# Performance work log

Hardware: AMD Instinct MI355X
Metric: run time of the kernel (lower is better)

Reference implementation:

```python
import jax, jax.numpy as jnp
import numpy as np

B, H, S, D = 2, 12, 4096, 768
BS = 64              # block size
HD = D // H          # head dim = 64
NB = S // BS         # 64 blocks
MC = 3               # max graph connections per block
PEN = -10000.0
RSQRT_D = 1.0 / np.sqrt(HD).astype(np.float32)


def setup_inputs() -> dict:
    key = jax.random.key(0)
    ks = jax.random.split(key, 6)
    hidden_states = jax.random.normal(ks[0], (B, S, D), jnp.float32)
    Wq = jax.random.normal(ks[1], (D, D), jnp.float32) * 0.02
    Wk = jax.random.normal(ks[2], (D, D), jnp.float32) * 0.02
    Wv = jax.random.normal(ks[3], (D, D), jnp.float32) * 0.02
    Wo = jax.random.normal(ks[4], (D, D), jnp.float32) * 0.02
    graph_attn = jax.random.randint(ks[5], (B, H, NB, MC), 0, NB, jnp.int32)
    return dict(
        hidden_states=hidden_states, Wq=Wq, Wk=Wk, Wv=Wv, Wo=Wo,
        band_mask=jnp.ones((B, 1, NB - 4, BS, 3 * BS), jnp.float32),
        from_mask=jnp.ones((B, 1, S, 1), jnp.float32),
        to_mask=jnp.ones((B, 1, 1, S), jnp.float32),
        from_blocked_mask=jnp.ones((B, NB, BS), jnp.float32),
        to_blocked_mask=jnp.ones((B, NB, BS), jnp.float32),
        graph_attn=graph_attn,
    )


def reference(hidden_states, Wq, Wk, Wv, Wo, band_mask, from_mask, to_mask,
              from_blocked_mask, to_blocked_mask, graph_attn):
    def proj(W):  # [B,S,D] -> [B,H,S,HD]
        return (hidden_states @ W.T).reshape(B, S, H, HD).transpose(0, 2, 1, 3)

    q, k, v = proj(Wq), proj(Wk), proj(Wv)
    bq = q.reshape(B, H, NB, BS, HD)
    bk = k.reshape(B, H, NB, BS, HD)
    bv = v.reshape(B, H, NB, BS, HD)

    # gather graph-selected key/value blocks: [B,H,NB,MC*BS,HD]
    gather = jax.vmap(jax.vmap(lambda blocks, idx: blocks[idx]))
    gk = gather(bk, graph_attn).reshape(B, H, NB, MC * BS, HD)
    gv = gather(bv, graph_attn).reshape(B, H, NB, MC * BS, HD)

    # graph mask from blocked masks: [B,H,NB,BS,MC*BS]
    gm = jax.vmap(lambda tm, ga: tm[ga])(to_blocked_mask, graph_attn)  # [B,H,NB,MC,BS]
    gm = gm.reshape(B, H, NB, MC * BS)
    graph_mask = jnp.einsum('blq,bhlk->bhlqk', from_blocked_mask, gm)

    # ---- first block: global attention over all keys ----
    fp = jnp.einsum('bhqd,bhkd->bhqk', bq[:, :, 0], k) * RSQRT_D + (1.0 - to_mask) * PEN
    first_ctx = jnp.einsum('bhqk,bhkd->bhqd', jax.nn.softmax(fp, -1), v)[:, :, None]

    # ---- second block: blocks 0,1,2,last + graph-gathered ----
    sk = jnp.concatenate([bk[:, :, 0], bk[:, :, 1], bk[:, :, 2], bk[:, :, -1], gk[:, :, 1]], axis=2)
    sv = jnp.concatenate([bv[:, :, 0], bv[:, :, 1], bv[:, :, 2], bv[:, :, -1], gv[:, :, 1]], axis=2)
    sp = jnp.einsum('bhqd,bhkd->bhqk', bq[:, :, 1], sk) * RSQRT_D
    seq_pad = jnp.concatenate([to_mask[:, :, :, :3 * BS], to_mask[:, :, :, -BS:],
                               jnp.ones((B, 1, 1, MC * BS), to_mask.dtype)], axis=3)
    rand_pad = jnp.concatenate([jnp.ones((B, H, BS, 4 * BS), graph_mask.dtype),
                                graph_mask[:, :, 1]], axis=3)
    sp = sp + (1.0 - jnp.minimum(seq_pad, rand_pad)) * PEN
    second_ctx = jnp.einsum('bhqk,bhkd->bhqd', jax.nn.softmax(sp, -1), sv)[:, :, None]

    # ---- middle blocks: sliding window (3 blocks) + first + last + graph ----
    ek = jnp.concatenate([bk[:, :, 1:-3], bk[:, :, 2:-2], bk[:, :, 3:-1]], axis=3)  # [B,H,NB-4,3BS,HD]
    ev = jnp.concatenate([bv[:, :, 1:-3], bv[:, :, 2:-2], bv[:, :, 3:-1]], axis=3)
    qm = bq[:, :, 2:-2]
    inner = jnp.einsum('bhlqd,bhlkd->bhlqk', qm, ek) * RSQRT_D + (1.0 - band_mask) * PEN
    randp = jnp.einsum('bhlqd,bhlkd->bhlqk', qm, gk[:, :, 2:-2]) * RSQRT_D + (1.0 - graph_mask[:, :, 2:-2]) * PEN
    firstp = jnp.einsum('bhlqd,bhkd->bhlqk', qm, bk[:, :, 0]) * RSQRT_D + (1.0 - to_mask[:, :, :, None, :BS]) * PEN
    lastp = jnp.einsum('bhlqd,bhkd->bhlqk', qm, bk[:, :, -1]) * RSQRT_D + (1.0 - to_mask[:, :, :, None, -BS:]) * PEN
    band = jnp.concatenate([firstp, inner, randp, lastp], axis=-1)
    attn = jax.nn.softmax(band, -1)
    mid_ctx = (jnp.einsum('bhlqk,bhlkd->bhlqd', attn[..., BS:4 * BS], ev)
               + jnp.einsum('bhlqk,bhlkd->bhlqd', attn[..., 4 * BS:4 * BS + MC * BS], gv[:, :, 2:-2])
               + jnp.einsum('bhlqk,bhkd->bhlqd', attn[..., :BS], bv[:, :, 0])
               + jnp.einsum('bhlqk,bhkd->bhlqd', attn[..., -BS:], bv[:, :, -1]))

    # ---- second-to-last block ----
    slk = jnp.concatenate([bk[:, :, 0], bk[:, :, -3], bk[:, :, -2], bk[:, :, -1], gk[:, :, -2]], axis=2)
    slv = jnp.concatenate([bv[:, :, 0], bv[:, :, -3], bv[:, :, -2], bv[:, :, -1], gv[:, :, -2]], axis=2)
    slp = jnp.einsum('bhqd,bhkd->bhqk', bq[:, :, -2], slk) * RSQRT_D
    sl_seq = jnp.concatenate([to_mask[:, :, :, :BS], to_mask[:, :, :, -3 * BS:],
                              jnp.ones((B, 1, 1, MC * BS), to_mask.dtype)], axis=3)
    sl_rand = jnp.concatenate([jnp.ones((B, H, BS, 4 * BS), graph_mask.dtype),
                               graph_mask[:, :, -2]], axis=3)
    slp = slp + (1.0 - jnp.minimum(sl_seq, sl_rand)) * PEN
    sl_ctx = jnp.einsum('bhqk,bhkd->bhqd', jax.nn.softmax(slp, -1), slv)[:, :, None]

    # ---- last block: global attention over all keys ----
    lp = jnp.einsum('bhqd,bhkd->bhqk', bq[:, :, -1], k) * RSQRT_D + (1.0 - to_mask) * PEN
    last_ctx = jnp.einsum('bhqk,bhkd->bhqd', jax.nn.softmax(lp, -1), v)[:, :, None]

    ctx = jnp.concatenate([first_ctx, second_ctx, mid_ctx, sl_ctx, last_ctx], axis=2)
    ctx = ctx.reshape(B, H, S, HD) * from_mask            # [B,H,S,HD]
    ctx = ctx.transpose(0, 2, 1, 3).reshape(B, S, D)      # [B,S,D]
    return ctx @ Wo.T                                     # output projection (no bias)
```

## Files before the change

### kernel.cpp

```cpp
#include <hip/hip_runtime.h>
#include <hip/hip_bf16.h>

#define BB 2
#define HH 12
#define SS 4096
#define DD 768
#define HD 64
#define NBK 64
#define MC 3

typedef __attribute__((ext_vector_type(8))) short short8_t;
typedef __attribute__((ext_vector_type(4))) float float4_t;

__device__ __forceinline__ unsigned short f2bf(float f) {
  union { float f; unsigned u; } c;
  c.f = f;
  unsigned u = c.u + 0x7FFFu + ((c.u >> 16) & 1u);
  return (unsigned short)(u >> 16);
}

__device__ __forceinline__ void gload16(const unsigned short* gp,
                                        unsigned short* lp) {
  __builtin_amdgcn_global_load_lds(
      (const __attribute__((address_space(1))) unsigned int*)gp,
      (__attribute__((address_space(3))) unsigned int*)lp, 16, 0, 0);
}

#define LDK 72

__global__ __launch_bounds__(256) void cvt_all(
    const float* __restrict__ hs, const float* __restrict__ Wq,
    const float* __restrict__ Wk, const float* __restrict__ Wv,
    const float* __restrict__ Wo, unsigned short* __restrict__ hsb,
    unsigned short* __restrict__ wqkvb, unsigned short* __restrict__ wob) {
  long i4 = (long)blockIdx.x * 256 + threadIdx.x;
  const float* src;
  unsigned short* dst;
  if (i4 < 1572864) {
    src = hs + i4 * 4;
    dst = hsb + i4 * 4;
  } else {
    long r = i4 - 1572864;
    int w = (int)(r / 147456);
    long e = r % 147456;
    src = (w == 0 ? Wq : w == 1 ? Wk : w == 2 ? Wv : Wo) + e * 4;
    dst = (w < 3) ? (wqkvb + (long)w * 589824 + e * 4) : (wob + e * 4);
  }
  float4_t v = *(const float4_t*)src;
  uint2 p;
  p.x = (unsigned)f2bf(v[0]) | ((unsigned)f2bf(v[1]) << 16);
  p.y = (unsigned)f2bf(v[2]) | ((unsigned)f2bf(v[3]) << 16);
  *(uint2*)dst = p;
}

#define STAGE_A(buf_, A_, m0_, kt_)                                           \
  {                                                                           \
    int rr_ = lane >> 3;                                                      \
    int cg_ = (lane & 7) ^ rr_;                                               \
    _Pragma("unroll") for (int u = 0; u < 4; u++) {                           \
      int g_ = w * 4 + u;                                                     \
      gload16(A_ + (size_t)(m0_ + g_ * 8 + rr_) * DD + kt_ + cg_ * 8,         \
              &As[buf_][g_ * 512]);                                           \
    }                                                                         \
  }

#define LOAD_FRAGS_AB(buf_, kt_, kk_)                                         \
  int cb = qd + ((kk_) >> 3);                                                 \
  short8_t af[4], bfr[4];                                                     \
  _Pragma("unroll") for (int i = 0; i < 4; i++) {                             \
    int r_ = wm + i * 16 + fr;                                                \
    af[i] = *(const short8_t*)&As[buf_][r_ * 64 + (cb ^ (fr & 7)) * 8];       \
  }                                                                           \
  _Pragma("unroll") for (int j = 0; j < 4; j++)                               \
    bfr[j] = *(const short8_t*)&Wg[(size_t)(j * 16) * DD + (kt_) + (kk_)];

__global__ __launch_bounds__(256) void gemm_qkv_b(
    const unsigned short* __restrict__ A, const unsigned short* __restrict__ W,
    unsigned short* __restrict__ qb, unsigned short* __restrict__ kb,
    unsigned short* __restrict__ vtb) {
  __shared__ unsigned short As[2][128 * 64];
  int tid = threadIdx.x;
  int m0 = blockIdx.x * 128;
  int n0 = blockIdx.y * 128;
  int lane = tid & 63;
  int w = tid >> 6;
  int wm = (w >> 1) * 64;
  int wn = (w & 1) * 64;
  int fr = lane & 15;
  int qd = lane >> 4;
  int ysel = n0 / 768;
  const unsigned short* Wg = W + (size_t)(n0 + wn + fr) * DD + qd * 8;

  float4_t acc[4][4];
#pragma unroll
  for (int i = 0; i < 4; i++)
#pragma unroll
    for (int j = 0; j < 4; j++)
#pragma unroll
      for (int r = 0; r < 4; r++) acc[i][j][r] = 0.f;

  STAGE_A(0, A, m0, 0)
  int p = 0;

  if (ysel < 2) {
    for (int kt = 0; kt < DD; kt += 64) {
      __syncthreads();
      if (kt + 64 < DD) STAGE_A(p ^ 1, A, m0, kt + 64)
#pragma unroll
      for (int kk = 0; kk < 64; kk += 32) {
        LOAD_FRAGS_AB(p, kt, kk)
#pragma unroll
        for (int i = 0; i < 4; i++)
#pragma unroll
          for (int j = 0; j < 4; j++)
            acc[j][i] = __builtin_amdgcn_mfma_f32_16x16x32_bf16(
                bfr[j], af[i], acc[j][i], 0, 0, 0);
      }
      p ^= 1;
    }
    int cn = lane & 15;
    int quad = lane >> 4;
    float scale = (ysel == 0) ? 0.125f : 1.0f;
    unsigned short* dst = (ysel == 0) ? qb : kb;
    int nb0 = n0 - ysel * 768;
#pragma unroll
    for (int j = 0; j < 4; j++)
#pragma unroll
      for (int i = 0; i < 4; i++) {
        int m = m0 + wm + i * 16 + cn;
        int nn = nb0 + wn + j * 16 + quad * 4;
        int b = m >> 12, s = m & 4095;
        int h = nn >> 6, d0 = nn & 63;
        uint2 pk;
        pk.x = (unsigned)f2bf(acc[j][i][0] * scale) |
               ((unsigned)f2bf(acc[j][i][1] * scale) << 16);
        pk.y = (unsigned)f2bf(acc[j][i][2] * scale) |
               ((unsigned)f2bf(acc[j][i][3] * scale) << 16);
        *(uint2*)&dst[(((size_t)b * HH + h) * SS + s) * HD + d0] = pk;
      }
  } else {
    for (int kt = 0; kt < DD; kt += 64) {
      __syncthreads();
      if (kt + 64 < DD) STAGE_A(p ^ 1, A, m0, kt + 64)
#pragma unroll
      for (int kk = 0; kk < 64; kk += 32) {
        LOAD_FRAGS_AB(p, kt, kk)
#pragma unroll
        for (int i = 0; i < 4; i++)
#pragma unroll
          for (int j = 0; j < 4; j++)
            acc[i][j] = __builtin_amdgcn_mfma_f32_16x16x32_bf16(
                af[i], bfr[j], acc[i][j], 0, 0, 0);
      }
      p ^= 1;
    }
    int cn = lane & 15;
    int quad = lane >> 4;
    int nb0 = n0 - 1536;
#pragma unroll
    for (int i = 0; i < 4; i++)
#pragma unroll
      for (int j = 0; j < 4; j++) {
        int m = m0 + wm + i * 16 + quad * 4;
        int nn = nb0 + wn + j * 16 + cn;
        int b = m >> 12, s0 = m & 4095;
        int h = nn >> 6, d = nn & 63;
        uint2 pk;
        pk.x = (unsigned)f2bf(acc[i][j][0]) |
               ((unsigned)f2bf(acc[i][j][1]) << 16);
        pk.y = (unsigned)f2bf(acc[i][j][2]) |
               ((unsigned)f2bf(acc[i][j][3]) << 16);
        *(uint2*)&vtb[(((size_t)b * HH + h) * HD + d) * SS + s0] = pk;
      }
  }
}

__global__ __launch_bounds__(256) void gemm_out_b(
    const unsigned short* __restrict__ A, const unsigned short* __restrict__ W,
    float* __restrict__ dst) {
  __shared__ unsigned short As[2][128 * 64];
  int tid = threadIdx.x;
  int m0 = blockIdx.x * 128;
  int n0 = blockIdx.y * 128;
  int lane = tid & 63;
  int w = tid >> 6;
  int wm = (w >> 1) * 64;
  int wn = (w & 1) * 64;
  int fr = lane & 15;
  int qd = lane >> 4;
  const unsigned short* Wg = W + (size_t)(n0 + wn + fr) * DD + qd * 8;

  float4_t acc[4][4];
#pragma unroll
  for (int i = 0; i < 4; i++)
#pragma unroll
    for (int j = 0; j < 4; j++)
#pragma unroll
      for (int r = 0; r < 4; r++) acc[i][j][r] = 0.f;

  STAGE_A(0, A, m0, 0)
  int p = 0;
  for (int kt = 0; kt < DD; kt += 64) {
    __syncthreads();
    if (kt + 64 < DD) STAGE_A(p ^ 1, A, m0, kt + 64)
#pragma unroll
    for (int kk = 0; kk < 64; kk += 32) {
      LOAD_FRAGS_AB(p, kt, kk)
#pragma unroll
      for (int i = 0; i < 4; i++)
#pragma unroll
        for (int j = 0; j < 4; j++)
          acc[i][j] = __builtin_amdgcn_mfma_f32_16x16x32_bf16(
              af[i], bfr[j], acc[i][j], 0, 0, 0);
    }
    p ^= 1;
  }

  int cn = lane & 15;
  int rb = (lane >> 4) * 4;
#pragma unroll
  for (int i = 0; i < 4; i++)
#pragma unroll
    for (int j = 0; j < 4; j++)
#pragma unroll
      for (int r = 0; r < 4; r++) {
        int m = m0 + wm + i * 16 + rb + r;
        int n = n0 + wn + j * 16 + cn;
        dst[(size_t)m * DD + n] = acc[i][j][r];
      }
}

__global__ __launch_bounds__(256) void attn2(
    const unsigned short* __restrict__ q, const unsigned short* __restrict__ k,
    const unsigned short* __restrict__ vt, const int* __restrict__ graph,
    unsigned short* __restrict__ ctxb, float* __restrict__ part) {
  __shared__ unsigned short Ks[2][64 * LDK];
  __shared__ unsigned short Vs[2][64 * LDK];
  __shared__ unsigned short Ps[4][16 * LDK];

  int tid = threadIdx.x;
  int id = blockIdx.x;
  int b, h, l, nkb, heavy, chunk = 0, hid = 0;
  int list[8];
  if (id < 384) {
    heavy = 1;
    hid = id >> 3;
    chunk = id & 7;
    b = hid / 24;
    int r = hid % 24;
    h = r >> 1;
    l = (r & 1) ? (NBK - 1) : 0;
    nkb = 8;
#pragma unroll
    for (int i = 0; i < 8; i++) list[i] = chunk * 8 + i;
  } else {
    heavy = 0;
    int j = id - 384;
    b = j / 744;
    int r = j % 744;
    h = r / 62;
    l = 1 + r % 62;
    const int* g = graph + (((size_t)b * HH + h) * NBK + l) * MC;
    int n = 0;
    if (l == 1) {
      list[0] = 0; list[1] = 1; list[2] = 2; list[3] = NBK - 1; n = 4;
    } else if (l == NBK - 2) {
      list[0] = 0; list[1] = NBK - 3; list[2] = NBK - 2; list[3] = NBK - 1; n = 4;
    } else {
      list[0] = 0; list[1] = l - 1; list[2] = l; list[3] = l + 1;
      list[4] = NBK - 1; n = 5;
    }
    for (int m = 0; m < MC; m++) list[n++] = g[m];
    nkb = n;
  }
  size_t base = ((size_t)b * HH + h) * SS * HD;

  int lane = tid & 63;
  int w = tid >> 6;
  int lr = lane & 15;
  int quad = lane >> 4;

  short8_t qa[2];
  {
    const unsigned short* qp =
        q + base + (size_t)(l * 64 + w * 16 + lr) * HD + quad * 8;
    qa[0] = *(const short8_t*)qp;
    qa[1] = *(const short8_t*)(qp + 32);
  }

  float4_t Ot[4];
  float ls[4];
#pragma unroll
  for (int t = 0; t < 4; t++)
#pragma unroll
    for (int r = 0; r < 4; r++) Ot[t][r] = 0.f;
#pragma unroll
  for (int r = 0; r < 4; r++) ls[r] = 0.f;

  int srow = tid >> 3;
  int scol = (tid & 7) * 8;

  uint4 kr0, kr1, vr0, vr1;
  {
    int kb = list[0];
    const unsigned short* kp = k + base + (size_t)(kb * 64 + srow) * HD + scol;
    const unsigned short* vp = vt + base + (size_t)srow * SS + kb * 64 + scol;
    kr0 = *(const uint4*)kp;
    kr1 = *(const uint4*)(kp + 32 * HD);
    vr0 = *(const uint4*)vp;
    vr1 = *(const uint4*)(vp + 32 * SS);
  }
  *(uint4*)&Ks[0][srow * LDK + scol] = kr0;
  *(uint4*)&Ks[0][(srow + 32) * LDK + scol] = kr1;
  *(uint4*)&Vs[0][srow * LDK + scol] = vr0;
  *(uint4*)&Vs[0][(srow + 32) * LDK + scol] = vr1;
  int p = 0;

  for (int t = 0; t < nkb; t++) {
    __syncthreads();

    if (t + 1 < nkb) {
      int kb = list[t + 1];
      const unsigned short* kp = k + base + (size_t)(kb * 64 + srow) * HD + scol;
      const unsigned short* vp = vt + base + (size_t)srow * SS + kb * 64 + scol;
      kr0 = *(const uint4*)kp;
      kr1 = *(const uint4*)(kp + 32 * HD);
      vr0 = *(const uint4*)vp;
      vr1 = *(const uint4*)(vp + 32 * SS);
    }

    float4_t st[4];
#pragma unroll
    for (int tt = 0; tt < 4; tt++) {
#pragma unroll
      for (int r = 0; r < 4; r++) st[tt][r] = 0.f;
      short8_t kb0 = *(const short8_t*)&Ks[p][(tt * 16 + lr) * LDK + quad * 8];
      short8_t kb1 =
          *(const short8_t*)&Ks[p][(tt * 16 + lr) * LDK + quad * 8 + 32];
      st[tt] = __builtin_amdgcn_mfma_f32_16x16x32_bf16(qa[0], kb0, st[tt], 0, 0, 0);
      st[tt] = __builtin_amdgcn_mfma_f32_16x16x32_bf16(qa[1], kb1, st[tt], 0, 0, 0);
    }

#pragma unroll
    for (int tt = 0; tt < 4; tt++)
#pragma unroll
      for (int r = 0; r < 4; r++) {
        float pv = __expf(st[tt][r]);
        st[tt][r] = pv;
        ls[r] += pv;
        Ps[w][(quad * 4 + r) * LDK + tt * 16 + lr] = f2bf(pv);
      }

#pragma unroll
    for (int s = 0; s < 2; s++) {
      short8_t pa = *(const short8_t*)&Ps[w][lr * LDK + s * 32 + quad * 8];
#pragma unroll
      for (int tt = 0; tt < 4; tt++) {
        short8_t vb =
            *(const short8_t*)&Vs[p][(tt * 16 + lr) * LDK + s * 32 + quad * 8];
        Ot[tt] = __builtin_amdgcn_mfma_f32_16x16x32_bf16(pa, vb, Ot[tt], 0, 0, 0);
      }
    }

    if (t + 1 < nkb) {
      *(uint4*)&Ks[p ^ 1][srow * LDK + scol] = kr0;
      *(uint4*)&Ks[p ^ 1][(srow + 32) * LDK + scol] = kr1;
      *(uint4*)&Vs[p ^ 1][srow * LDK + scol] = vr0;
      *(uint4*)&Vs[p ^ 1][(srow + 32) * LDK + scol] = vr1;
    }
    p ^= 1;
  }

#pragma unroll
  for (int r = 0; r < 4; r++)
#pragma unroll
    for (int off = 1; off < 16; off <<= 1) ls[r] += __shfl_xor(ls[r], off);

  if (!heavy) {
#pragma unroll
    for (int r = 0; r < 4; r++) {
      float inv = 1.f / ls[r];
      size_t row = (size_t)b * SS + (size_t)l * 64 + w * 16 + quad * 4 + r;
#pragma unroll
      for (int tt = 0; tt < 4; tt++)
        ctxb[row * DD + h * HD + tt * 16 + lr] = f2bf(Ot[tt][r] * inv);
    }
  } else {
    float* pb = part + ((size_t)hid * 8 + chunk) * 4160;
#pragma unroll
    for (int r = 0; r < 4; r++) {
      int rowi = w * 16 + quad * 4 + r;
#pragma unroll
      for (int tt = 0; tt < 4; tt++)
        pb[rowi * 64 + tt * 16 + lr] = Ot[tt][r];
      if (lr == 0) pb[4096 + rowi] = ls[r];
    }
  }
}

__global__ __launch_bounds__(256) void reduce_heavy(
    const float* __restrict__ part, unsigned short* __restrict__ ctxb) {
  __shared__ float lrow[64];
  int hid = blockIdx.x;
  int tid = threadIdx.x;
  int b = hid / 24;
  int r = hid % 24;
  int h = r >> 1;
  int l = (r & 1) ? (NBK - 1) : 0;
  const float* pb = part + (size_t)hid * 8 * 4160;
  if (tid < 64) {
    float s = 0.f;
#pragma unroll
    for (int c = 0; c < 8; c++) s += pb[c * 4160 + 4096 + tid];
    lrow[tid] = s;
  }
  __syncthreads();
#pragma unroll
  for (int e = tid; e < 4096; e += 256) {
    float o = 0.f;
#pragma unroll
    for (int c = 0; c < 8; c++) o += pb[c * 4160 + e];
    int rowi = e >> 6, col = e & 63;
    size_t row = (size_t)b * SS + (size_t)l * 64 + rowi;
    ctxb[row * DD + h * HD + col] = f2bf(o / lrow[rowi]);
  }
}

extern "C" void kernel_launch(void* const* d_in, const int* in_sizes, int n_in,
                              void* d_out, int out_size, void* d_ws,
                              size_t ws_size, hipStream_t stream) {
  const float* hs = (const float*)d_in[0];
  const float* Wq = (const float*)d_in[1];
  const float* Wk = (const float*)d_in[2];
  const float* Wv = (const float*)d_in[3];
  const float* Wo = (const float*)d_in[4];
  const int* graph = (const int*)d_in[10];

  const size_t NHS = (size_t)BB * SS * DD;
  unsigned short* hsb = (unsigned short*)d_ws;
  unsigned short* wqkvb = hsb + NHS;
  unsigned short* wob = wqkvb + 3 * 768 * 768;
  unsigned short* qb = wob + 768 * 768;
  unsigned short* kb = qb + NHS;
  unsigned short* vtb = kb + NHS;
  unsigned short* ctxb = vtb + NHS;
  float* part = (float*)(ctxb + NHS);

  cvt_all<<<8448, 256, 0, stream>>>(hs, Wq, Wk, Wv, Wo, hsb, wqkvb, wob);
  gemm_qkv_b<<<dim3(64, 18, 1), 256, 0, stream>>>(hsb, wqkvb, qb, kb, vtb);
  attn2<<<1872, 256, 0, stream>>>(qb, kb, vtb, graph, ctxb, part);
  reduce_heavy<<<48, 256, 0, stream>>>(part, ctxb);
  gemm_out_b<<<dim3(64, 6, 1), 256, 0, stream>>>(ctxb, wob, (float*)d_out);
}
```

Before: 242.8 us.

## Stage both GEMM operands through LDS with a triple-buffered async pipeline

Both projection GEMMs now stage the weight tile in LDS alongside the activation tile, where before the weights were read straight from global memory into registers. The K loop becomes a 3-stage ring of 32-wide K slices, each prefetched two steps ahead with async global-to-LDS loads. Partial vmcnt waits plus a raw barrier replace __syncthreads so the loads overlap the MFMA work. This aims to hide global latency and cut uncoalesced weight loads, at the cost of more LDS, twice as many barrier rounds, and reliance on exact waitcnt accounting.

```diff
diff --git a/kernel.cpp b/kernel.cpp
--- a/kernel.cpp
+++ b/kernel.cpp
@@ -53,32 +53,63 @@
   *(uint2*)dst = p;
 }
 
-#define STAGE_A(buf_, A_, m0_, kt_)                                           \
-  {                                                                           \
-    int rr_ = lane >> 3;                                                      \
-    int cg_ = (lane & 7) ^ rr_;                                               \
-    _Pragma("unroll") for (int u = 0; u < 4; u++) {                           \
-      int g_ = w * 4 + u;                                                     \
-      gload16(A_ + (size_t)(m0_ + g_ * 8 + rr_) * DD + kt_ + cg_ * 8,         \
-              &As[buf_][g_ * 512]);                                           \
-    }                                                                         \
-  }
-
-#define LOAD_FRAGS_AB(buf_, kt_, kk_)                                         \
-  int cb = qd + ((kk_) >> 3);                                                 \
-  short8_t af[4], bfr[4];                                                     \
-  _Pragma("unroll") for (int i = 0; i < 4; i++) {                             \
-    int r_ = wm + i * 16 + fr;                                                \
-    af[i] = *(const short8_t*)&As[buf_][r_ * 64 + (cb ^ (fr & 7)) * 8];       \
-  }                                                                           \
-  _Pragma("unroll") for (int j = 0; j < 4; j++)                               \
-    bfr[j] = *(const short8_t*)&Wg[(size_t)(j * 16) * DD + (kt_) + (kk_)];
+#define BOUND4()                                                           \
+  do {                                                                     \
+    asm volatile("s_waitcnt vmcnt(4) lgkmcnt(0)" ::: "memory");            \
+    __builtin_amdgcn_s_barrier();                                          \
+    asm volatile("" ::: "memory");                                         \
+  } while (0)
+#define BOUND0()                                                           \
+  do {                                                                     \
+    asm volatile("s_waitcnt vmcnt(0) lgkmcnt(0)" ::: "memory");            \
+    __builtin_amdgcn_s_barrier();                                          \
+    asm volatile("" ::: "memory");                                         \
+  } while (0)
+
+#define STAGE3(s_, kt_)                                                    \
+  {                                                                        \
+    gload16(Ag + (kt_), &As[s_][wbase]);                                   \
+    gload16(Ag + (kt_) + 64 * DD, &As[s_][wbase + 2048]);                  \
+    gload16(Bg + (kt_), &Bs[s_][wbase]);                                   \
+    gload16(Bg + (kt_) + 64 * DD, &Bs[s_][wbase + 2048]);                  \
+  }
+
+#define KLOOP3(MM)                                                         \
+  STAGE3(0, 0)                                                             \
+  STAGE3(1, 32)                                                            \
+  int sl = 0;                                                              \
+  for (int T = 0; T < 24; T++) {                                           \
+    if (T == 23) { BOUND0(); } else { BOUND4(); }                          \
+    if (T + 2 < 24) {                                                      \
+      int s2 = sl + 2;                                                     \
+      if (s2 >= 3) s2 -= 3;                                                \
+      STAGE3(s2, (T + 2) * 32)                                             \
+    }                                                                      \
+    short8_t af[4], bfr[4];                                                \
+    _Pragma("unroll") for (int i = 0; i < 4; i++)                          \
+        af[i] = *(const short8_t*)&As[sl][(wm + i * 16 + fr) * 32 +        \
+                                          fslot * 8];                      \
+    _Pragma("unroll") for (int j = 0; j < 4; j++)                          \
+        bfr[j] = *(const short8_t*)&Bs[sl][(wn + j * 16 + fr) * 32 +       \
+                                           fslot * 8];                     \
+    _Pragma("unroll") for (int i = 0; i < 4; i++)                          \
+        _Pragma("unroll") for (int j = 0; j < 4; j++) { MM(i, j) }         \
+    sl = (sl == 2) ? 0 : sl + 1;                                           \
+  }
+
+#define MMQK(i, j)                                                         \
+  acc[j][i] = __builtin_amdgcn_mfma_f32_16x16x32_bf16(bfr[j], af[i],       \
+                                                      acc[j][i], 0, 0, 0);
+#define MMN(i, j)                                                          \
+  acc[i][j] = __builtin_amdgcn_mfma_f32_16x16x32_bf16(af[i], bfr[j],       \
+                                                      acc[i][j], 0, 0, 0);
 
 __global__ __launch_bounds__(256) void gemm_qkv_b(
     const unsigned short* __restrict__ A, const unsigned short* __restrict__ W,
     unsigned short* __restrict__ qb, unsigned short* __restrict__ kb,
     unsigned short* __restrict__ vtb) {
-  __shared__ unsigned short As[2][128 * 64];
+  __shared__ unsigned short As[3][128 * 32];
+  __shared__ unsigned short Bs[3][128 * 32];
   int tid = threadIdx.x;
   int m0 = blockIdx.x * 128;
   int n0 = blockIdx.y * 128;
@@ -88,8 +119,13 @@
   int wn = (w & 1) * 64;
   int fr = lane & 15;
   int qd = lane >> 4;
+  int fslot = qd ^ (fr & 3) ^ ((fr >> 2) & 3);
+  int srow = w * 16 + (lane >> 2);
+  int scg = (lane & 3) ^ ((lane >> 2) & 3) ^ ((lane >> 4) & 3);
+  int wbase = w * 512;
+  const unsigned short* Ag = A + (size_t)(m0 + srow) * DD + scg * 8;
+  const unsigned short* Bg = W + (size_t)(n0 + srow) * DD + scg * 8;
   int ysel = n0 / 768;
-  const unsigned short* Wg = W + (size_t)(n0 + wn + fr) * DD + qd * 8;
 
   float4_t acc[4][4];
 #pragma unroll
@@ -99,25 +135,8 @@
 #pragma unroll
       for (int r = 0; r < 4; r++) acc[i][j][r] = 0.f;
 
-  STAGE_A(0, A, m0, 0)
-  int p = 0;
-
   if (ysel < 2) {
-    for (int kt = 0; kt < DD; kt += 64) {
-      __syncthreads();
-      if (kt + 64 < DD) STAGE_A(p ^ 1, A, m0, kt + 64)
-#pragma unroll
-      for (int kk = 0; kk < 64; kk += 32) {
-        LOAD_FRAGS_AB(p, kt, kk)
-#pragma unroll
-        for (int i = 0; i < 4; i++)
-#pragma unroll
-          for (int j = 0; j < 4; j++)
-            acc[j][i] = __builtin_amdgcn_mfma_f32_16x16x32_bf16(
-                bfr[j], af[i], acc[j][i], 0, 0, 0);
-      }
-      p ^= 1;
-    }
+    KLOOP3(MMQK)
     int cn = lane & 15;
     int quad = lane >> 4;
     float scale = (ysel == 0) ? 0.125f : 1.0f;
@@ -139,21 +158,7 @@
         *(uint2*)&dst[(((size_t)b * HH + h) * SS + s) * HD + d0] = pk;
       }
   } else {
-    for (int kt = 0; kt < DD; kt += 64) {
-      __syncthreads();
-      if (kt + 64 < DD) STAGE_A(p ^ 1, A, m0, kt + 64)
-#pragma unroll
-      for (int kk = 0; kk < 64; kk += 32) {
-        LOAD_FRAGS_AB(p, kt, kk)
-#pragma unroll
-        for (int i = 0; i < 4; i++)
-#pragma unroll
-          for (int j = 0; j < 4; j++)
-            acc[i][j] = __builtin_amdgcn_mfma_f32_16x16x32_bf16(
-                af[i], bfr[j], acc[i][j], 0, 0, 0);
-      }
-      p ^= 1;
-    }
+    KLOOP3(MMN)
     int cn = lane & 15;
     int quad = lane >> 4;
     int nb0 = n0 - 1536;
@@ -178,7 +183,8 @@
 __global__ __launch_bounds__(256) void gemm_out_b(
     const unsigned short* __restrict__ A, const unsigned short* __restrict__ W,
     float* __restrict__ dst) {
-  __shared__ unsigned short As[2][128 * 64];
+  __shared__ unsigned short As[3][128 * 32];
+  __shared__ unsigned short Bs[3][128 * 32];
   int tid = threadIdx.x;
   int m0 = blockIdx.x * 128;
   int n0 = blockIdx.y * 128;
@@ -188,7 +194,12 @@
   int wn = (w & 1) * 64;
   int fr = lane & 15;
   int qd = lane >> 4;
-  const unsigned short* Wg = W + (size_t)(n0 + wn + fr) * DD + qd * 8;
+  int fslot = qd ^ (fr & 3) ^ ((fr >> 2) & 3);
+  int srow = w * 16 + (lane >> 2);
+  int scg = (lane & 3) ^ ((lane >> 2) & 3) ^ ((lane >> 4) & 3);
+  int wbase = w * 512;
+  const unsigned short* Ag = A + (size_t)(m0 + srow) * DD + scg * 8;
+  const unsigned short* Bg = W + (size_t)(n0 + srow) * DD + scg * 8;
 
   float4_t acc[4][4];
 #pragma unroll
@@ -198,23 +209,7 @@
 #pragma unroll
       for (int r = 0; r < 4; r++) acc[i][j][r] = 0.f;
 
-  STAGE_A(0, A, m0, 0)
-  int p = 0;
-  for (int kt = 0; kt < DD; kt += 64) {
-    __syncthreads();
-    if (kt + 64 < DD) STAGE_A(p ^ 1, A, m0, kt + 64)
-#pragma unroll
-    for (int kk = 0; kk < 64; kk += 32) {
-      LOAD_FRAGS_AB(p, kt, kk)
-#pragma unroll
-      for (int i = 0; i < 4; i++)
-#pragma unroll
-        for (int j = 0; j < 4; j++)
-          acc[i][j] = __builtin_amdgcn_mfma_f32_16x16x32_bf16(
-              af[i], bfr[j], acc[i][j], 0, 0, 0);
-    }
-    p ^= 1;
-  }
+  KLOOP3(MMN)
 
   int cn = lane & 15;
   int rb = (lane >> 4) * 4;
```

New measurement: 219.0 us. 1.11x faster.

## Stage weight tiles in LDS and shrink GEMM N-tile to 64

Applied to the files above, without the earlier changes.

Both projection GEMMs now copy the weight (B) tile into shared memory with async global-to-LDS loads and double-buffering, where before each wave read its fragments straight from global memory. The N tile drops from 128 to 64 and each wave now owns a 32-row M slice, which doubles the grid size and halves the accumulators per thread. This targets the latency of the direct global B loads and low block counts (384 blocks for the output GEMM), at the cost of less reuse of A per block and more LDS use.

```diff
diff --git a/kernel.cpp b/kernel.cpp
--- a/kernel.cpp
+++ b/kernel.cpp
@@ -53,7 +53,7 @@
   *(uint2*)dst = p;
 }
 
-#define STAGE_A(buf_, A_, m0_, kt_)                                           \
+#define STAGE_T(buf_, A_, B_, m0_, n0_, kt_)                                  \
   {                                                                           \
     int rr_ = lane >> 3;                                                      \
     int cg_ = (lane & 7) ^ rr_;                                               \
@@ -62,59 +62,63 @@
       gload16(A_ + (size_t)(m0_ + g_ * 8 + rr_) * DD + kt_ + cg_ * 8,         \
               &As[buf_][g_ * 512]);                                           \
     }                                                                         \
-  }
-
-#define LOAD_FRAGS_AB(buf_, kt_, kk_)                                         \
+    _Pragma("unroll") for (int u = 0; u < 2; u++) {                           \
+      int g_ = w * 2 + u;                                                     \
+      gload16(B_ + (size_t)(n0_ + g_ * 8 + rr_) * DD + kt_ + cg_ * 8,         \
+              &Bs[buf_][g_ * 512]);                                           \
+    }                                                                         \
+  }
+
+#define LOAD_FRAGS2(buf_, kk_)                                                \
   int cb = qd + ((kk_) >> 3);                                                 \
-  short8_t af[4], bfr[4];                                                     \
-  _Pragma("unroll") for (int i = 0; i < 4; i++) {                             \
+  short8_t af[2], bfr[4];                                                     \
+  _Pragma("unroll") for (int i = 0; i < 2; i++) {                             \
     int r_ = wm + i * 16 + fr;                                                \
     af[i] = *(const short8_t*)&As[buf_][r_ * 64 + (cb ^ (fr & 7)) * 8];       \
   }                                                                           \
-  _Pragma("unroll") for (int j = 0; j < 4; j++)                               \
-    bfr[j] = *(const short8_t*)&Wg[(size_t)(j * 16) * DD + (kt_) + (kk_)];
+  _Pragma("unroll") for (int j = 0; j < 4; j++) {                             \
+    int r_ = j * 16 + fr;                                                     \
+    bfr[j] = *(const short8_t*)&Bs[buf_][r_ * 64 + (cb ^ (fr & 7)) * 8];      \
+  }
 
 __global__ __launch_bounds__(256) void gemm_qkv_b(
     const unsigned short* __restrict__ A, const unsigned short* __restrict__ W,
     unsigned short* __restrict__ qb, unsigned short* __restrict__ kb,
     unsigned short* __restrict__ vtb) {
   __shared__ unsigned short As[2][128 * 64];
+  __shared__ unsigned short Bs[2][64 * 64];
   int tid = threadIdx.x;
   int m0 = blockIdx.x * 128;
-  int n0 = blockIdx.y * 128;
+  int n0 = blockIdx.y * 64;
   int lane = tid & 63;
   int w = tid >> 6;
-  int wm = (w >> 1) * 64;
-  int wn = (w & 1) * 64;
+  int wm = w * 32;
   int fr = lane & 15;
   int qd = lane >> 4;
   int ysel = n0 / 768;
-  const unsigned short* Wg = W + (size_t)(n0 + wn + fr) * DD + qd * 8;
-
-  float4_t acc[4][4];
-#pragma unroll
-  for (int i = 0; i < 4; i++)
-#pragma unroll
-    for (int j = 0; j < 4; j++)
-#pragma unroll
-      for (int r = 0; r < 4; r++) acc[i][j][r] = 0.f;
-
-  STAGE_A(0, A, m0, 0)
+
+  float4_t acc[8];
+#pragma unroll
+  for (int i = 0; i < 8; i++)
+#pragma unroll
+    for (int r = 0; r < 4; r++) acc[i][r] = 0.f;
+
+  STAGE_T(0, A, W, m0, n0, 0)
   int p = 0;
 
   if (ysel < 2) {
     for (int kt = 0; kt < DD; kt += 64) {
       __syncthreads();
-      if (kt + 64 < DD) STAGE_A(p ^ 1, A, m0, kt + 64)
+      if (kt + 64 < DD) STAGE_T(p ^ 1, A, W, m0, n0, kt + 64)
 #pragma unroll
       for (int kk = 0; kk < 64; kk += 32) {
-        LOAD_FRAGS_AB(p, kt, kk)
-#pragma unroll
-        for (int i = 0; i < 4; i++)
+        LOAD_FRAGS2(p, kk)
+#pragma unroll
+        for (int i = 0; i < 2; i++)
 #pragma unroll
           for (int j = 0; j < 4; j++)
-            acc[j][i] = __builtin_amdgcn_mfma_f32_16x16x32_bf16(
-                bfr[j], af[i], acc[j][i], 0, 0, 0);
+            acc[j * 2 + i] = __builtin_amdgcn_mfma_f32_16x16x32_bf16(
+                bfr[j], af[i], acc[j * 2 + i], 0, 0, 0);
       }
       p ^= 1;
     }
@@ -126,31 +130,31 @@
 #pragma unroll
     for (int j = 0; j < 4; j++)
 #pragma unroll
-      for (int i = 0; i < 4; i++) {
+      for (int i = 0; i < 2; i++) {
         int m = m0 + wm + i * 16 + cn;
-        int nn = nb0 + wn + j * 16 + quad * 4;
+        int nn = nb0 + j * 16 + quad * 4;
         int b = m >> 12, s = m & 4095;
         int h = nn >> 6, d0 = nn & 63;
         uint2 pk;
-        pk.x = (unsigned)f2bf(acc[j][i][0] * scale) |
-               ((unsigned)f2bf(acc[j][i][1] * scale) << 16);
-        pk.y = (unsigned)f2bf(acc[j][i][2] * scale) |
-               ((unsigned)f2bf(acc[j][i][3] * scale) << 16);
+        pk.x = (unsigned)f2bf(acc[j * 2 + i][0] * scale) |
+               ((unsigned)f2bf(acc[j * 2 + i][1] * scale) << 16);
+        pk.y = (unsigned)f2bf(acc[j * 2 + i][2] * scale) |
+               ((unsigned)f2bf(acc[j * 2 + i][3] * scale) << 16);
         *(uint2*)&dst[(((size_t)b * HH + h) * SS + s) * HD + d0] = pk;
       }
   } else {
     for (int kt = 0; kt < DD; kt += 64) {
       __syncthreads();
-      if (kt + 64 < DD) STAGE_A(p ^ 1, A, m0, kt + 64)
+      if (kt + 64 < DD) STAGE_T(p ^ 1, A, W, m0, n0, kt + 64)
 #pragma unroll
       for (int kk = 0; kk < 64; kk += 32) {
-        LOAD_FRAGS_AB(p, kt, kk)
-#pragma unroll
-        for (int i = 0; i < 4; i++)
+        LOAD_FRAGS2(p, kk)
+#pragma unroll
+        for (int i = 0; i < 2; i++)
 #pragma unroll
           for (int j = 0; j < 4; j++)
-            acc[i][j] = __builtin_amdgcn_mfma_f32_16x16x32_bf16(
-                af[i], bfr[j], acc[i][j], 0, 0, 0);
+            acc[i * 4 + j] = __builtin_amdgcn_mfma_f32_16x16x32_bf16(
+                af[i], bfr[j], acc[i * 4 + j], 0, 0, 0);
       }
       p ^= 1;
     }
@@ -158,18 +162,18 @@
     int quad = lane >> 4;
     int nb0 = n0 - 1536;
 #pragma unroll
-    for (int i = 0; i < 4; i++)
+    for (int i = 0; i < 2; i++)
 #pragma unroll
       for (int j = 0; j < 4; j++) {
         int m = m0 + wm + i * 16 + quad * 4;
-        int nn = nb0 + wn + j * 16 + cn;
+        int nn = nb0 + j * 16 + cn;
         int b = m >> 12, s0 = m & 4095;
         int h = nn >> 6, d = nn & 63;
         uint2 pk;
-        pk.x = (unsigned)f2bf(acc[i][j][0]) |
-               ((unsigned)f2bf(acc[i][j][1]) << 16);
-        pk.y = (unsigned)f2bf(acc[i][j][2]) |
-               ((unsigned)f2bf(acc[i][j][3]) << 16);
+        pk.x = (unsigned)f2bf(acc[i * 4 + j][0]) |
+               ((unsigned)f2bf(acc[i * 4 + j][1]) << 16);
+        pk.y = (unsigned)f2bf(acc[i * 4 + j][2]) |
+               ((unsigned)f2bf(acc[i * 4 + j][3]) << 16);
         *(uint2*)&vtb[(((size_t)b * HH + h) * HD + d) * SS + s0] = pk;
       }
   }
@@ -179,39 +183,36 @@
     const unsigned short* __restrict__ A, const unsigned short* __restrict__ W,
     float* __restrict__ dst) {
   __shared__ unsigned short As[2][128 * 64];
+  __shared__ unsigned short Bs[2][64 * 64];
   int tid = threadIdx.x;
   int m0 = blockIdx.x * 128;
-  int n0 = blockIdx.y * 128;
+  int n0 = blockIdx.y * 64;
   int lane = tid & 63;
   int w = tid >> 6;
-  int wm = (w >> 1) * 64;
-  int wn = (w & 1) * 64;
+  int wm = w * 32;
   int fr = lane & 15;
   int qd = lane >> 4;
-  const unsigned short* Wg = W + (size_t)(n0 + wn + fr) * DD + qd * 8;
-
-  float4_t acc[4][4];
-#pragma unroll
-  for (int i = 0; i < 4; i++)
-#pragma unroll
-    for (int j = 0; j < 4; j++)
-#pragma unroll
-      for (int r = 0; r < 4; r++) acc[i][j][r] = 0.f;
-
-  STAGE_A(0, A, m0, 0)
+
+  float4_t acc[8];
+#pragma unroll
+  for (int i = 0; i < 8; i++)
+#pragma unroll
+    for (int r = 0; r < 4; r++) acc[i][r] = 0.f;
+
+  STAGE_T(0, A, W, m0, n0, 0)
   int p = 0;
   for (int kt = 0; kt < DD; kt += 64) {
     __syncthreads();
-    if (kt + 64 < DD) STAGE_A(p ^ 1, A, m0, kt + 64)
+    if (kt + 64 < DD) STAGE_T(p ^ 1, A, W, m0, n0, kt + 64)
 #pragma unroll
     for (int kk = 0; kk < 64; kk += 32) {
-      LOAD_FRAGS_AB(p, kt, kk)
-#pragma unroll
-      for (int i = 0; i < 4; i++)
+      LOAD_FRAGS2(p, kk)
+#pragma unroll
+      for (int i = 0; i < 2; i++)
 #pragma unroll
         for (int j = 0; j < 4; j++)
-          acc[i][j] = __builtin_amdgcn_mfma_f32_16x16x32_bf16(
-              af[i], bfr[j], acc[i][j], 0, 0, 0);
+          acc[i * 4 + j] = __builtin_amdgcn_mfma_f32_16x16x32_bf16(
+              af[i], bfr[j], acc[i * 4 + j], 0, 0, 0);
     }
     p ^= 1;
   }
@@ -219,14 +220,14 @@
   int cn = lane & 15;
   int rb = (lane >> 4) * 4;
 #pragma unroll
-  for (int i = 0; i < 4; i++)
+  for (int i = 0; i < 2; i++)
 #pragma unroll
     for (int j = 0; j < 4; j++)
 #pragma unroll
       for (int r = 0; r < 4; r++) {
         int m = m0 + wm + i * 16 + rb + r;
-        int n = n0 + wn + j * 16 + cn;
-        dst[(size_t)m * DD + n] = acc[i][j][r];
+        int n = n0 + j * 16 + cn;
+        dst[(size_t)m * DD + n] = acc[i * 4 + j][r];
       }
 }
 
@@ -447,8 +448,8 @@
   float* part = (float*)(ctxb + NHS);
 
   cvt_all<<<8448, 256, 0, stream>>>(hs, Wq, Wk, Wv, Wo, hsb, wqkvb, wob);
-  gemm_qkv_b<<<dim3(64, 18, 1), 256, 0, stream>>>(hsb, wqkvb, qb, kb, vtb);
+  gemm_qkv_b<<<dim3(64, 36, 1), 256, 0, stream>>>(hsb, wqkvb, qb, kb, vtb);
   attn2<<<1872, 256, 0, stream>>>(qb, kb, vtb, graph, ctxb, part);
   reduce_heavy<<<48, 256, 0, stream>>>(part, ctxb);
-  gemm_out_b<<<dim3(64, 6, 1), 256, 0, stream>>>(ctxb, wob, (float*)d_out);
-}
+  gemm_out_b<<<dim3(64, 12, 1), 256, 0, stream>>>(ctxb, wob, (float*)d_out);
+}
```

Measured after the change: 209.5 us. 13.7% less time.
